# Kernel tuning notes

Hardware: AMD Instinct MI355X
Metric: run time of the kernel (lower is better)

The kernel has to match this reference:

```python
import jax, jax.numpy as jnp
import numpy as np

B, C, H, W = 64, 1024, 16, 16
R = 8            # ratio
CK = C // R      # key channels
N = H * W


def setup_inputs() -> dict:
    key = jax.random.key(0)
    ks = jax.random.split(key, 12)
    g = 0.02  # xavier gain used in the module
    def xav(k, fan_out, fan_in):
        std = g * (2.0 / (fan_in + fan_out)) ** 0.5
        return jax.random.normal(k, (fan_out, fan_in), dtype=jnp.float32) * std
    return {
        "x": jax.random.normal(ks[0], (B, C, H, W), dtype=jnp.float32),
        "y": jax.random.normal(ks[1], (B, C, H, W), dtype=jnp.float32),
        "wk1": xav(ks[2], CK, C),
        "bk1": jnp.zeros((CK,), jnp.float32),
        "wk2": xav(ks[3], CK, C),
        "bk2": jnp.zeros((CK,), jnp.float32),
        "wv1": xav(ks[4], C, C),
        "bv1": jnp.zeros((C,), jnp.float32),
        "wv2": xav(ks[5], C, C),
        "bv2": jnp.zeros((C,), jnp.float32),
        "gamma1": jnp.zeros((1,), jnp.float32),
        "gamma2": jnp.zeros((1,), jnp.float32),
    }


def reference(x, y, wk1, bk1, wk2, bk2, wv1, bv1, wv2, bv2, gamma1, gamma2):
    b, c, h, w = x.shape
    n = h * w
    xf = x.reshape(b, c, n)  # [B,C,N]
    yf = y.reshape(b, c, n)
    # 1x1 convs as channel GEMMs
    kx = jnp.einsum('oc,bcn->bon', wk1, xf) + bk1[:, None]  # [B,CK,N]
    ky = jnp.einsum('oc,bcn->bon', wk2, yf) + bk2[:, None]
    vx = jnp.einsum('oc,bcn->bon', wv1, xf) + bv1[:, None]  # [B,C,N]
    vy = jnp.einsum('oc,bcn->bon', wv2, yf) + bv2[:, None]
    # cross energies: query = permuted key projection of own branch
    energy_x = jnp.einsum('bkn,bkm->bnm', kx, ky)  # q_x @ k_y
    energy_y = jnp.einsum('bkn,bkm->bnm', ky, kx)  # q_y @ k_x
    attn_x = jax.nn.softmax(energy_x, axis=-1)  # [B,N,N]
    attn_y = jax.nn.softmax(energy_y, axis=-1)
    # out = V @ attn^T
    ox = jnp.einsum('bcn,bmn->bcm', vx, attn_x).reshape(b, c, h, w)
    oy = jnp.einsum('bcn,bmn->bcm', vy, attn_y).reshape(b, c, h, w)
    out_x = gamma1 * ox + x
    out_y = gamma2 * oy + y
    return out_x, out_y
```

## Files before the change

### kernel.cpp

```cpp
#include <hip/hip_runtime.h>
#include <hip/hip_bf16.h>
#include <stdint.h>

#define B_  64
#define C_  1024
#define CK_ 128
#define N_  256

typedef __bf16 bf16;
typedef __attribute__((ext_vector_type(8))) __bf16 bf16x8;
typedef __attribute__((ext_vector_type(4))) __bf16 bf16x4;
typedef __attribute__((ext_vector_type(4))) float floatx4;

constexpr size_t OFF_XBT = 0;
constexpr size_t OFF_YBT = 33554432;
constexpr size_t OFF_WK1 = 67108864;
constexpr size_t OFF_WK2 = 67371008;
constexpr size_t OFF_WV1 = 67633152;
constexpr size_t OFF_WV2 = 69730304;
constexpr size_t OFF_AX  = 71827456;
constexpr size_t OFF_AY  = 80216064;
constexpr size_t WS_NEEDED = 88604672;

__device__ __forceinline__ void async16(const void* g, void* l) {
  __builtin_amdgcn_global_load_lds((const __attribute__((address_space(1))) void*)g,
                                   (__attribute__((address_space(3))) void*)l, 16, 0, 0);
}

__global__ __launch_bounds__(256) void k_xpose(const float* __restrict__ xin,
                                               const float* __restrict__ yin,
                                               bf16* __restrict__ xo, bf16* __restrict__ yo) {
  __shared__ float tile[64][65];
  int nt = blockIdx.x, ct = blockIdx.y, z = blockIdx.z;
  int b = z & 63;
  const float* in = (z < 64) ? xin : yin;
  bf16* out = (z < 64) ? xo : yo;
  const float* src = in + (size_t)b * C_ * N_ + (size_t)ct * 64 * N_ + nt * 64;
  bf16* dst = out + (size_t)b * N_ * C_ + (size_t)nt * 64 * C_ + ct * 64;
  int c4 = (threadIdx.x & 15) * 4, r0 = threadIdx.x >> 4;
#pragma unroll
  for (int i = 0; i < 4; ++i) {
    int r = r0 + i * 16;
    float4 v = *(const float4*)(src + r * N_ + c4);
    tile[r][c4 + 0] = v.x; tile[r][c4 + 1] = v.y;
    tile[r][c4 + 2] = v.z; tile[r][c4 + 3] = v.w;
  }
  __syncthreads();
#pragma unroll
  for (int i = 0; i < 4; ++i) {
    int r = r0 + i * 16;
    bf16x4 o;
    o[0] = (bf16)tile[c4 + 0][r]; o[1] = (bf16)tile[c4 + 1][r];
    o[2] = (bf16)tile[c4 + 2][r]; o[3] = (bf16)tile[c4 + 3][r];
    *(bf16x4*)(dst + (size_t)r * C_ + c4) = o;
  }
}

__global__ __launch_bounds__(256) void k_cvt2(const float* __restrict__ inA,
                                              const float* __restrict__ inB,
                                              bf16* __restrict__ outA, bf16* __restrict__ outB,
                                              int n4each) {
  int i = blockIdx.x * 256 + threadIdx.x;
  const float* in = (i < n4each) ? inA : inB;
  bf16* out = (i < n4each) ? outA : outB;
  int j = (i < n4each) ? i : (i - n4each);
  if (i < 2 * n4each) {
    float4 v = ((const float4*)in)[j];
    bf16x4 o;
    o[0] = (bf16)v.x; o[1] = (bf16)v.y; o[2] = (bf16)v.z; o[3] = (bf16)v.w;
    ((bf16x4*)out)[j] = o;
  }
}

template <int KITERS>
__device__ __forceinline__ void gemm128_core(const bf16* __restrict__ Ag, int ldA,
                                             const bf16* __restrict__ Bg, int ldB,
                                             char* smem, floatx4 (&acc)[4][4]) {
  const int tid = threadIdx.x;
  const int l = tid & 63, wid = tid >> 6;
  const int wm = wid & 1, wn = wid >> 1;
  auto issue = [&](int kt, int buf) {
    const int k0 = kt * 32;
#pragma unroll
    for (int s = 0; s < 2; ++s) {
      int row = (s << 6) + (wid << 4) + (l >> 2);
      int q = (l & 3) ^ ((row >> 1) & 3);
      async16(Ag + (size_t)row * ldA + k0 + q * 8, smem + buf * 8192 + (s << 12) + (wid << 10));
      async16(Bg + (size_t)row * ldB + k0 + q * 8, smem + 24576 + buf * 8192 + (s << 12) + (wid << 10));
    }
  };
  auto compute = [&](int buf) {
    const char* As = smem + buf * 8192;
    const char* Bs = smem + 24576 + buf * 8192;
    bf16x8 af[4], bfr[4];
#pragma unroll
    for (int t = 0; t < 4; ++t) {
      int m = (wm << 6) + t * 16 + (l & 15);
      af[t] = *(const bf16x8*)(As + m * 64 + (((l >> 4) ^ ((m >> 1) & 3)) << 4));
      int n = (wn << 6) + t * 16 + (l & 15);
      bfr[t] = *(const bf16x8*)(Bs + n * 64 + (((l >> 4) ^ ((n >> 1) & 3)) << 4));
    }
#pragma unroll
    for (int tm = 0; tm < 4; ++tm)
#pragma unroll
      for (int tn = 0; tn < 4; ++tn)
        acc[tm][tn] = __builtin_amdgcn_mfma_f32_16x16x32_bf16(af[tm], bfr[tn], acc[tm][tn], 0, 0, 0);
  };
  issue(0, 0);
  if (KITERS > 1) issue(1, 1);
#pragma unroll
  for (int kt = 0; kt < KITERS; ++kt) {
    if (kt + 1 < KITERS) asm volatile("s_waitcnt vmcnt(4) lgkmcnt(0)" ::: "memory");
    else                 asm volatile("s_waitcnt vmcnt(0) lgkmcnt(0)" ::: "memory");
    __builtin_amdgcn_s_barrier();
    asm volatile("" ::: "memory");
    if (kt + 2 < KITERS) issue(kt + 2, (kt + 2) % 3);
    __builtin_amdgcn_s_setprio(1);
    compute(kt % 3);
    __builtin_amdgcn_s_setprio(0);
  }
}

__global__ __launch_bounds__(256) void k_projk(
    const bf16* __restrict__ xbT, const bf16* __restrict__ ybT,
    const bf16* __restrict__ wk1b, const bf16* __restrict__ wk2b,
    const float* __restrict__ bk1, const float* __restrict__ bk2,
    bf16* __restrict__ kxT, bf16* __restrict__ kyT) {
  __shared__ __align__(16) char smem[49152];
  int mt = blockIdx.x, br = blockIdx.y, b = blockIdx.z;
  const bf16* A = (br ? ybT : xbT) + (size_t)b * N_ * C_ + (size_t)mt * 128 * C_;
  const bf16* Bt = br ? wk2b : wk1b;
  const float* bias = br ? bk2 : bk1;
  bf16* out = (br ? kyT : kxT) + (size_t)b * N_ * CK_ + (size_t)mt * 128 * CK_;
  floatx4 acc[4][4];
  floatx4 z = {0.f, 0.f, 0.f, 0.f};
#pragma unroll
  for (int i = 0; i < 4; ++i)
#pragma unroll
    for (int j = 0; j < 4; ++j) acc[i][j] = z;
  gemm128_core<32>(A, C_, Bt, C_, smem, acc);
  const int l = threadIdx.x & 63, wid = threadIdx.x >> 6;
  const int wm = wid & 1, wn = wid >> 1;
#pragma unroll
  for (int tn = 0; tn < 4; ++tn) {
    int oc = (wn << 6) + tn * 16 + (l & 15);
    float bkv = bias[oc];
#pragma unroll
    for (int tm = 0; tm < 4; ++tm)
#pragma unroll
      for (int r = 0; r < 4; ++r) {
        int row = (wm << 6) + tm * 16 + ((l >> 4) << 2) + r;
        out[row * CK_ + oc] = (bf16)(acc[tm][tn][r] + bkv);
      }
  }
}

__global__ __launch_bounds__(256) void k_esoft(
    const bf16* __restrict__ kxT, const bf16* __restrict__ kyT,
    bf16* __restrict__ ax, bf16* __restrict__ ay) {
  int rh = blockIdx.x, br = blockIdx.y, b = blockIdx.z;
  const bf16* A  = (br ? kyT : kxT) + (size_t)b * N_ * CK_;
  const bf16* Bm = (br ? kxT : kyT) + (size_t)b * N_ * CK_;
  bf16* outp = (br ? ay : ax) + (size_t)b * N_ * N_;
  const int tid = threadIdx.x, l = tid & 63, wid = tid >> 6;
  const int m0 = rh * 128 + wid * 32;

  floatx4 acc[2][16];
  floatx4 z = {0.f, 0.f, 0.f, 0.f};
#pragma unroll
  for (int i = 0; i < 2; ++i)
#pragma unroll
    for (int j = 0; j < 16; ++j) acc[i][j] = z;

#pragma unroll
  for (int kk = 0; kk < 4; ++kk) {
    bf16x8 af[2];
    const bf16* pa = A + (size_t)(m0 + (l & 15)) * CK_ + kk * 32 + ((l >> 4) << 3);
    af[0] = *(const bf16x8*)(pa);
    af[1] = *(const bf16x8*)(pa + 16 * CK_);
#pragma unroll
    for (int h = 0; h < 2; ++h) {
      bf16x8 bfr[8];
#pragma unroll
      for (int t = 0; t < 8; ++t) {
        int n = (h * 8 + t) * 16 + (l & 15);
        bfr[t] = *(const bf16x8*)(Bm + (size_t)n * CK_ + kk * 32 + ((l >> 4) << 3));
      }
#pragma unroll
      for (int tm = 0; tm < 2; ++tm)
#pragma unroll
        for (int t = 0; t < 8; ++t)
          acc[tm][h * 8 + t] =
              __builtin_amdgcn_mfma_f32_16x16x32_bf16(af[tm], bfr[t], acc[tm][h * 8 + t], 0, 0, 0);
    }
  }

#pragma unroll
  for (int tm = 0; tm < 2; ++tm)
#pragma unroll
    for (int r = 0; r < 4; ++r) {
      float mx = -1e30f;
#pragma unroll
      for (int tn = 0; tn < 16; ++tn) mx = fmaxf(mx, acc[tm][tn][r]);
#pragma unroll
      for (int off = 8; off > 0; off >>= 1) mx = fmaxf(mx, __shfl_xor(mx, off));
      float s = 0.f;
#pragma unroll
      for (int tn = 0; tn < 16; ++tn) {
        float e = __expf(acc[tm][tn][r] - mx);
        acc[tm][tn][r] = e;
        s += e;
      }
#pragma unroll
      for (int off = 8; off > 0; off >>= 1) s += __shfl_xor(s, off);
      float rc = 1.0f / s;
      int m = m0 + tm * 16 + ((l >> 4) << 2) + r;
#pragma unroll
      for (int tn = 0; tn < 16; ++tn)
        outp[(size_t)m * N_ + tn * 16 + (l & 15)] = (bf16)(acc[tm][tn][r] * rc);
    }
}

__global__ __launch_bounds__(256, 3) void k_vapply(
    const bf16* __restrict__ xbT, const bf16* __restrict__ ybT,
    const bf16* __restrict__ wv1b, const bf16* __restrict__ wv2b,
    const float* __restrict__ bv1, const float* __restrict__ bv2,
    const bf16* __restrict__ ax, const bf16* __restrict__ ay,
    const float* __restrict__ xin0, const float* __restrict__ yin0,
    const float* __restrict__ g1, const float* __restrict__ g2,
    float* __restrict__ out) {
  __shared__ __align__(16) char smem[49152];
  int id = blockIdx.x;
  int xcd = id & 7;
  int idx = id >> 3;
  int b = xcd + ((idx >> 5) << 3);
  int inner = idx & 31;
  int ct = inner & 15, br = inner >> 4;

  const bf16* A1 = (br ? wv2b : wv1b) + (size_t)ct * 64 * C_;
  const bf16* Bt1 = (br ? ybT : xbT) + (size_t)b * N_ * C_;
  const float* bias = br ? bv2 : bv1;
  const bf16* attn = (br ? ay : ax) + (size_t)b * N_ * N_;
  const float* xin = (br ? yin0 : xin0) + (size_t)b * C_ * N_ + (size_t)ct * 64 * N_;
  float gamma = br ? g2[0] : g1[0];
  float* o = out + (size_t)br * B_ * C_ * N_ + (size_t)b * C_ * N_ + (size_t)ct * 64 * N_;
  const int tid = threadIdx.x, l = tid & 63, wid = tid >> 6;

  auto loadA = [&](int kt, bf16x8 (&af)[4]) {
    const bf16* p = A1 + (size_t)(l & 15) * C_ + kt * 32 + ((l >> 4) << 3);
#pragma unroll
    for (int t = 0; t < 4; ++t) af[t] = *(const bf16x8*)(p + (size_t)t * 16 * C_);
  };
  auto issueB = [&](int kt, int buf) {
    const int k0 = kt * 32;
#pragma unroll
    for (int s = 0; s < 4; ++s) {
      int row = (s << 6) + (wid << 4) + (l >> 2);
      int q = (l & 3) ^ ((row >> 1) & 3);
      async16(Bt1 + (size_t)row * C_ + k0 + q * 8, smem + buf * 16384 + (s << 12) + (wid << 10));
    }
  };
  floatx4 acc[4][4];
  floatx4 z = {0.f, 0.f, 0.f, 0.f};
#pragma unroll
  for (int i = 0; i < 4; ++i)
#pragma unroll
    for (int j = 0; j < 4; ++j) acc[i][j] = z;

  auto compute1 = [&](int buf, bf16x8 (&af)[4]) {
    const char* Bs = smem + buf * 16384;
    bf16x8 bfr[4];
#pragma unroll
    for (int t = 0; t < 4; ++t) {
      int n = (wid << 6) + t * 16 + (l & 15);
      bfr[t] = *(const bf16x8*)(Bs + n * 64 + (((l >> 4) ^ ((n >> 1) & 3)) << 4));
    }
#pragma unroll
    for (int tm = 0; tm < 4; ++tm)
#pragma unroll
      for (int tn = 0; tn < 4; ++tn)
        acc[tm][tn] = __builtin_amdgcn_mfma_f32_16x16x32_bf16(af[tm], bfr[tn], acc[tm][tn], 0, 0, 0);
  };

  bf16x8 afA[4], afB[4], afC[4];
  issueB(0, 0); loadA(0, afA);
  issueB(1, 1); loadA(1, afB);
  auto step = [&](int kt, int buf, bf16x8 (&afU)[4], bf16x8 (&afN)[4], bool more1, bool more2) {
    if (more1) asm volatile("s_waitcnt vmcnt(8) lgkmcnt(0)" ::: "memory");
    else       asm volatile("s_waitcnt vmcnt(0) lgkmcnt(0)" ::: "memory");
    __builtin_amdgcn_s_barrier();
    asm volatile("" ::: "memory");
    if (more2) { issueB(kt + 2, (buf + 2) % 3); loadA(kt + 2, afN); }
    __builtin_amdgcn_s_setprio(1);
    compute1(buf, afU);
    __builtin_amdgcn_s_setprio(0);
  };
  for (int kt = 0; kt < 30; kt += 3) {
    step(kt,     0, afA, afC, true, true);
    step(kt + 1, 1, afB, afA, true, true);
    step(kt + 2, 2, afC, afB, true, true);
  }
  step(30, 0, afA, afC, true, false);
  step(31, 1, afB, afA, false, false);
  __syncthreads();

  char* vt = smem;
#pragma unroll
  for (int tm = 0; tm < 4; ++tm)
#pragma unroll
    for (int r = 0; r < 4; ++r) {
      int rr = tm * 16 + ((l >> 4) << 2) + r;
      float bkv = bias[ct * 64 + rr];
#pragma unroll
      for (int tn = 0; tn < 4; ++tn) {
        int n = (wid << 6) + tn * 16 + (l & 15);
        int ch = (n >> 3) ^ (rr & 7);
        *(bf16*)(vt + rr * 512 + ch * 16 + ((n & 7) << 1)) = (bf16)(acc[tm][tn][r] + bkv);
      }
    }

  auto loadB2 = [&](int kt, bf16x8 (&bb)[4]) {
    const bf16* p = attn + (size_t)((wid << 6) + (l & 15)) * N_ + kt * 32 + ((l >> 4) << 3);
#pragma unroll
    for (int t = 0; t < 4; ++t) bb[t] = *(const bf16x8*)(p + (size_t)t * 16 * N_);
  };
  auto compute2 = [&](int kt, bf16x8 (&bb)[4]) {
    bf16x8 af[4];
#pragma unroll
    for (int t = 0; t < 4; ++t) {
      int m = t * 16 + (l & 15);
      int ch = ((kt << 2) + (l >> 4)) ^ (m & 7);
      af[t] = *(const bf16x8*)(vt + m * 512 + (ch << 4));
    }
#pragma unroll
    for (int tm = 0; tm < 4; ++tm)
#pragma unroll
      for (int tn = 0; tn < 4; ++tn)
        acc[tm][tn] = __builtin_amdgcn_mfma_f32_16x16x32_bf16(af[tm], bb[tn], acc[tm][tn], 0, 0, 0);
  };

  bf16x8 bfA[4], bfB[4];
  loadB2(0, bfA);
  __syncthreads();
#pragma unroll
  for (int i = 0; i < 4; ++i)
#pragma unroll
    for (int j = 0; j < 4; ++j) acc[i][j] = z;
  for (int kt = 0; kt < 8; kt += 2) {
    loadB2(kt + 1, bfB);
    compute2(kt, bfA);
    if (kt + 2 < 8) loadB2(kt + 2, bfA);
    compute2(kt + 1, bfB);
  }

#pragma unroll
  for (int tm = 0; tm < 4; ++tm)
#pragma unroll
    for (int tn = 0; tn < 4; ++tn)
#pragma unroll
      for (int r = 0; r < 4; ++r) {
        int rr = tm * 16 + ((l >> 4) << 2) + r;
        int m = (wid << 6) + tn * 16 + (l & 15);
        int idx2 = rr * N_ + m;
        o[idx2] = gamma * acc[tm][tn][r] + xin[idx2];
      }
}

__global__ __launch_bounds__(256) void k_fallback(const float4* __restrict__ x,
                                                  const float4* __restrict__ y,
                                                  float4* __restrict__ out) {
  size_t i = (size_t)blockIdx.x * 256 + threadIdx.x;
  out[i] = x[i];
  out[4194304 + i] = y[i];
}

extern "C" void kernel_launch(void* const* d_in, const int* in_sizes, int n_in,
                              void* d_out, int out_size, void* d_ws, size_t ws_size,
                              hipStream_t stream) {
  const float* x   = (const float*)d_in[0];
  const float* y   = (const float*)d_in[1];
  const float* wk1 = (const float*)d_in[2];
  const float* bk1 = (const float*)d_in[3];
  const float* wk2 = (const float*)d_in[4];
  const float* bk2 = (const float*)d_in[5];
  const float* wv1 = (const float*)d_in[6];
  const float* bv1 = (const float*)d_in[7];
  const float* wv2 = (const float*)d_in[8];
  const float* bv2 = (const float*)d_in[9];
  const float* g1  = (const float*)d_in[10];
  const float* g2  = (const float*)d_in[11];
  float* out = (float*)d_out;

  if (ws_size < WS_NEEDED) {
    k_fallback<<<16384, 256, 0, stream>>>((const float4*)x, (const float4*)y, (float4*)out);
    return;
  }

  char* ws = (char*)d_ws;
  bf16* xbT  = (bf16*)(ws + OFF_XBT);
  bf16* ybT  = (bf16*)(ws + OFF_YBT);
  bf16* wk1b = (bf16*)(ws + OFF_WK1);
  bf16* wk2b = (bf16*)(ws + OFF_WK2);
  bf16* wv1b = (bf16*)(ws + OFF_WV1);
  bf16* wv2b = (bf16*)(ws + OFF_WV2);
  bf16* axp  = (bf16*)(ws + OFF_AX);
  bf16* ayp  = (bf16*)(ws + OFF_AY);
  bf16* kxT = (bf16*)((char*)out + (size_t)B_ * C_ * N_ * 4);
  bf16* kyT = (bf16*)((char*)out + (size_t)B_ * C_ * N_ * 4 + 4194304);

  k_xpose<<<dim3(4, 16, 128), 256, 0, stream>>>(x, y, xbT, ybT);
  k_cvt2<<<256, 256, 0, stream>>>(wk1, wk2, wk1b, wk2b, 32768);
  k_cvt2<<<2048, 256, 0, stream>>>(wv1, wv2, wv1b, wv2b, 262144);
  k_projk<<<dim3(2, 2, 64), 256, 0, stream>>>(xbT, ybT, wk1b, wk2b, bk1, bk2, kxT, kyT);
  k_esoft<<<dim3(2, 2, 64), 256, 0, stream>>>(kxT, kyT, axp, ayp);
  k_vapply<<<2048, 256, 0, stream>>>(xbT, ybT, wv1b, wv2b, bv1, bv2,
                                     axp, ayp, x, y, g1, g2, out);
}
```

Before: 494.8 us.

## Enlarge vapply tile to 128x256 with 8 waves and LDS-staged weights

k_vapply now gives each 512-thread block a 128-channel by 256-position tile, so the grid has 1024 blocks instead of 2048. Each block streams the bf16 activation operand once for twice as many output channels, halving reads of that operand. The weight operand is now loaded asynchronously into double-buffered LDS instead of straight into registers, and the activation buffers stay triple-buffered in 64KB of LDS. The risk is the __launch_bounds__(512, 4) hint: with 64 accumulator floats per thread, the register budget it implies may cause spills. LDS use also caps how many blocks can be resident per CU.

```diff
diff --git a/kernel.cpp b/kernel.cpp
--- a/kernel.cpp
+++ b/kernel.cpp
@@ -221,7 +221,7 @@
     }
 }
 
-__global__ __launch_bounds__(256, 3) void k_vapply(
+__global__ __launch_bounds__(512, 4) void k_vapply(
     const bf16* __restrict__ xbT, const bf16* __restrict__ ybT,
     const bf16* __restrict__ wv1b, const bf16* __restrict__ wv2b,
     const float* __restrict__ bv1, const float* __restrict__ bv2,
@@ -229,35 +229,36 @@
     const float* __restrict__ xin0, const float* __restrict__ yin0,
     const float* __restrict__ g1, const float* __restrict__ g2,
     float* __restrict__ out) {
-  __shared__ __align__(16) char smem[49152];
+  __shared__ __align__(16) char smem[65536];
   int id = blockIdx.x;
   int xcd = id & 7;
   int idx = id >> 3;
-  int b = xcd + ((idx >> 5) << 3);
-  int inner = idx & 31;
-  int ct = inner & 15, br = inner >> 4;
-
-  const bf16* A1 = (br ? wv2b : wv1b) + (size_t)ct * 64 * C_;
+  int b = xcd + ((idx >> 4) << 3);
+  int inner = idx & 15;
+  int ct = inner & 7, br = inner >> 3;
+
+  const bf16* A1 = (br ? wv2b : wv1b) + (size_t)ct * 128 * C_;
   const bf16* Bt1 = (br ? ybT : xbT) + (size_t)b * N_ * C_;
   const float* bias = br ? bv2 : bv1;
   const bf16* attn = (br ? ay : ax) + (size_t)b * N_ * N_;
-  const float* xin = (br ? yin0 : xin0) + (size_t)b * C_ * N_ + (size_t)ct * 64 * N_;
+  const float* xin = (br ? yin0 : xin0) + (size_t)b * C_ * N_ + (size_t)ct * 128 * N_;
   float gamma = br ? g2[0] : g1[0];
-  float* o = out + (size_t)br * B_ * C_ * N_ + (size_t)b * C_ * N_ + (size_t)ct * 64 * N_;
+  float* o = out + (size_t)br * B_ * C_ * N_ + (size_t)b * C_ * N_ + (size_t)ct * 128 * N_;
   const int tid = threadIdx.x, l = tid & 63, wid = tid >> 6;
-
-  auto loadA = [&](int kt, bf16x8 (&af)[4]) {
-    const bf16* p = A1 + (size_t)(l & 15) * C_ + kt * 32 + ((l >> 4) << 3);
-#pragma unroll
-    for (int t = 0; t < 4; ++t) af[t] = *(const bf16x8*)(p + (size_t)t * 16 * C_);
-  };
-  auto issueB = [&](int kt, int buf) {
-    const int k0 = kt * 32;
-#pragma unroll
-    for (int s = 0; s < 4; ++s) {
-      int row = (s << 6) + (wid << 4) + (l >> 2);
+  const int wm = wid >> 2, wn = wid & 3;
+
+  auto issueA = [&](int kt, int abuf) {
+    int row = (wid << 4) + (l >> 2);
+    int q = (l & 3) ^ ((row >> 1) & 3);
+    async16(A1 + (size_t)row * C_ + kt * 32 + q * 8, smem + abuf * 8192 + (wid << 10));
+  };
+  auto issueB = [&](int kt, int bbuf) {
+#pragma unroll
+    for (int s = 0; s < 2; ++s) {
+      int row = (s << 7) + (wid << 4) + (l >> 2);
       int q = (l & 3) ^ ((row >> 1) & 3);
-      async16(Bt1 + (size_t)row * C_ + k0 + q * 8, smem + buf * 16384 + (s << 12) + (wid << 10));
+      async16(Bt1 + (size_t)row * C_ + kt * 32 + q * 8,
+              smem + 16384 + bbuf * 16384 + (s << 13) + (wid << 10));
     }
   };
   floatx4 acc[4][4];
@@ -267,12 +268,15 @@
 #pragma unroll
     for (int j = 0; j < 4; ++j) acc[i][j] = z;
 
-  auto compute1 = [&](int buf, bf16x8 (&af)[4]) {
-    const char* Bs = smem + buf * 16384;
-    bf16x8 bfr[4];
+  auto compute1 = [&](int abuf, int bbuf) {
+    const char* As = smem + abuf * 8192;
+    const char* Bs = smem + 16384 + bbuf * 16384;
+    bf16x8 af[4], bfr[4];
 #pragma unroll
     for (int t = 0; t < 4; ++t) {
-      int n = (wid << 6) + t * 16 + (l & 15);
+      int m = (wm << 6) + t * 16 + (l & 15);
+      af[t] = *(const bf16x8*)(As + m * 64 + (((l >> 4) ^ ((m >> 1) & 3)) << 4));
+      int n = (wn << 6) + t * 16 + (l & 15);
       bfr[t] = *(const bf16x8*)(Bs + n * 64 + (((l >> 4) ^ ((n >> 1) & 3)) << 4));
     }
 #pragma unroll
@@ -282,26 +286,19 @@
         acc[tm][tn] = __builtin_amdgcn_mfma_f32_16x16x32_bf16(af[tm], bfr[tn], acc[tm][tn], 0, 0, 0);
   };
 
-  bf16x8 afA[4], afB[4], afC[4];
-  issueB(0, 0); loadA(0, afA);
-  issueB(1, 1); loadA(1, afB);
-  auto step = [&](int kt, int buf, bf16x8 (&afU)[4], bf16x8 (&afN)[4], bool more1, bool more2) {
-    if (more1) asm volatile("s_waitcnt vmcnt(8) lgkmcnt(0)" ::: "memory");
-    else       asm volatile("s_waitcnt vmcnt(0) lgkmcnt(0)" ::: "memory");
+  issueA(0, 0); issueB(0, 0); issueB(1, 1);
+#pragma unroll
+  for (int kt = 0; kt < 32; ++kt) {
+    if (kt < 31) asm volatile("s_waitcnt vmcnt(2) lgkmcnt(0)" ::: "memory");
+    else         asm volatile("s_waitcnt vmcnt(0) lgkmcnt(0)" ::: "memory");
     __builtin_amdgcn_s_barrier();
     asm volatile("" ::: "memory");
-    if (more2) { issueB(kt + 2, (buf + 2) % 3); loadA(kt + 2, afN); }
+    if (kt < 31) issueA(kt + 1, (kt + 1) & 1);
+    if (kt < 30) issueB(kt + 2, (kt + 2) % 3);
     __builtin_amdgcn_s_setprio(1);
-    compute1(buf, afU);
+    compute1(kt & 1, kt % 3);
     __builtin_amdgcn_s_setprio(0);
-  };
-  for (int kt = 0; kt < 30; kt += 3) {
-    step(kt,     0, afA, afC, true, true);
-    step(kt + 1, 1, afB, afA, true, true);
-    step(kt + 2, 2, afC, afB, true, true);
-  }
-  step(30, 0, afA, afC, true, false);
-  step(31, 1, afB, afA, false, false);
+  }
   __syncthreads();
 
   char* vt = smem;
@@ -309,18 +306,18 @@
   for (int tm = 0; tm < 4; ++tm)
 #pragma unroll
     for (int r = 0; r < 4; ++r) {
-      int rr = tm * 16 + ((l >> 4) << 2) + r;
-      float bkv = bias[ct * 64 + rr];
+      int rr = (wm << 6) + tm * 16 + ((l >> 4) << 2) + r;
+      float bkv = bias[ct * 128 + rr];
 #pragma unroll
       for (int tn = 0; tn < 4; ++tn) {
-        int n = (wid << 6) + tn * 16 + (l & 15);
+        int n = (wn << 6) + tn * 16 + (l & 15);
         int ch = (n >> 3) ^ (rr & 7);
         *(bf16*)(vt + rr * 512 + ch * 16 + ((n & 7) << 1)) = (bf16)(acc[tm][tn][r] + bkv);
       }
     }
 
   auto loadB2 = [&](int kt, bf16x8 (&bb)[4]) {
-    const bf16* p = attn + (size_t)((wid << 6) + (l & 15)) * N_ + kt * 32 + ((l >> 4) << 3);
+    const bf16* p = attn + (size_t)((wn << 6) + (l & 15)) * N_ + kt * 32 + ((l >> 4) << 3);
 #pragma unroll
     for (int t = 0; t < 4; ++t) bb[t] = *(const bf16x8*)(p + (size_t)t * 16 * N_);
   };
@@ -328,7 +325,7 @@
     bf16x8 af[4];
 #pragma unroll
     for (int t = 0; t < 4; ++t) {
-      int m = t * 16 + (l & 15);
+      int m = (wm << 6) + t * 16 + (l & 15);
       int ch = ((kt << 2) + (l >> 4)) ^ (m & 7);
       af[t] = *(const bf16x8*)(vt + m * 512 + (ch << 4));
     }
@@ -359,8 +356,8 @@
     for (int tn = 0; tn < 4; ++tn)
 #pragma unroll
       for (int r = 0; r < 4; ++r) {
-        int rr = tm * 16 + ((l >> 4) << 2) + r;
-        int m = (wid << 6) + tn * 16 + (l & 15);
+        int rr = (wm << 6) + tm * 16 + ((l >> 4) << 2) + r;
+        int m = (wn << 6) + tn * 16 + (l & 15);
         int idx2 = rr * N_ + m;
         o[idx2] = gamma * acc[tm][tn][r] + xin[idx2];
       }
@@ -413,6 +410,6 @@
   k_cvt2<<<2048, 256, 0, stream>>>(wv1, wv2, wv1b, wv2b, 262144);
   k_projk<<<dim3(2, 2, 64), 256, 0, stream>>>(xbT, ybT, wk1b, wk2b, bk1, bk2, kxT, kyT);
   k_esoft<<<dim3(2, 2, 64), 256, 0, stream>>>(kxT, kyT, axp, ayp);
-  k_vapply<<<2048, 256, 0, stream>>>(xbT, ybT, wv1b, wv2b, bv1, bv2,
+  k_vapply<<<1024, 512, 0, stream>>>(xbT, ybT, wv1b, wv2b, bv1, bv2,
                                      axp, ayp, x, y, g1, g2, out);
 }
```

After: 415.5 us. 16.0% less time.
